# Optimization experiments

Hardware: AMD Instinct MI355X
Metric: run time of the kernel (lower is better)

Reference implementation:

```python
import jax, jax.numpy as jnp
import numpy as np


def setup_inputs() -> dict:
    key = jax.random.key(0)
    k1, k2, k3 = jax.random.split(key, 3)
    B, C, D, H, W = 4, 64, 32, 64, 64
    x = jax.random.normal(k1, (B, C, D, H, W), dtype=jnp.float32)
    # Conv3d(in=2, out=1, k=7), PyTorch default init: U(-s, s), s = 1/sqrt(fan_in)
    fan_in = 2 * 7 * 7 * 7
    s = 1.0 / np.sqrt(fan_in)
    conv_w = jax.random.uniform(k2, (1, 2, 7, 7, 7), dtype=jnp.float32, minval=-s, maxval=s)
    conv_b = jax.random.uniform(k3, (1,), dtype=jnp.float32, minval=-s, maxval=s)
    return {"x": x, "conv_w": conv_w, "conv_b": conv_b}


def reference(x, conv_w, conv_b):
    # channel-wise max and mean -> [B, 2, D, H, W]
    xc = jnp.stack([jnp.max(x, axis=1), jnp.mean(x, axis=1)], axis=1)
    # conv3d 2->1, k7, stride 1, padding 3 (SAME)
    y = jax.lax.conv_general_dilated(
        xc, conv_w,
        window_strides=(1, 1, 1),
        padding=[(3, 3), (3, 3), (3, 3)],
        dimension_numbers=("NCDHW", "OIDHW", "NCDHW"),
    ) + conv_b[None, :, None, None, None]
    scale = jax.nn.sigmoid(y)  # [B, 1, D, H, W]
    return x * scale
```

## Files before the change

kernel.cpp:

```cpp
#include <hip/hip_runtime.h>
#include <math.h>

#define B_ 4
#define C_ 64
#define D_ 32
#define H_ 64
#define W_ 64
#define S_ (D_*H_*W_)
#define S4_ (S_/4)

typedef float floatx4 __attribute__((ext_vector_type(4)));

__global__ __launch_bounds__(256) void reduce_kernel(const float* __restrict__ x,
                                                     float* __restrict__ xc) {
    int i  = blockIdx.x * 256 + threadIdx.x;
    int b  = i >> 15;
    int s4 = i & (S4_ - 1);
    const float4* x4 = reinterpret_cast<const float4*>(x) + (size_t)b * C_ * S4_ + s4;
    float4 v = x4[0];
    float mx0 = v.x, mx1 = v.y, mx2 = v.z, mx3 = v.w;
    float sm0 = v.x, sm1 = v.y, sm2 = v.z, sm3 = v.w;
    #pragma unroll 8
    for (int c = 1; c < C_; ++c) {
        float4 t = x4[(size_t)c * S4_];
        mx0 = fmaxf(mx0, t.x); sm0 += t.x;
        mx1 = fmaxf(mx1, t.y); sm1 += t.y;
        mx2 = fmaxf(mx2, t.z); sm2 += t.z;
        mx3 = fmaxf(mx3, t.w); sm3 += t.w;
    }
    float4* o = reinterpret_cast<float4*>(xc);
    float4 a; a.x = mx0; a.y = mx1; a.z = mx2; a.w = mx3;
    o[((size_t)b * 2 + 0) * S4_ + s4] = a;
    const float inv = 1.0f / 64.0f;
    float4 m; m.x = sm0 * inv; m.y = sm1 * inv; m.z = sm2 * inv; m.w = sm3 * inv;
    o[((size_t)b * 2 + 1) * S4_ + s4] = m;
}

#define YS 72
#define ZS (10*YS)
#define CHS (10*ZS)
__global__ __launch_bounds__(256) void conv_gate_kernel(const float* __restrict__ xc,
                                                        const float* __restrict__ x,
                                                        const float* __restrict__ cw,
                                                        const float* __restrict__ cb,
                                                        float* __restrict__ out) {
    __shared__ float tile[2 * CHS];
    __shared__ float wl[784];

    const int tid = threadIdx.x;
    const int b  = blockIdx.z >> 3;
    const int d0 = (blockIdx.z & 7) * 4;
    const int h0 = blockIdx.y * 4;

    const int w4 = tid & 15;
    const int hh = (tid >> 4) & 3;
    const int dd = tid >> 6;

    for (int idx = tid; idx < 784; idx += 256) {
        int ch = idx / 392;
        int r  = idx - ch * 392;
        int kz = r / 56;
        int r2 = r - kz * 56;
        int ky = r2 >> 3;
        int kw = r2 & 7;
        wl[idx] = (kw < 7) ? cw[ch * 343 + kz * 49 + ky * 7 + kw] : 0.f;
    }
    for (int idx = tid; idx < 2 * 10 * 10 * 70; idx += 256) {
        int ch = idx / 7000;
        int r  = idx - ch * 7000;
        int z  = r / 700;
        int r2 = r - z * 700;
        int y  = r2 / 70;
        int xw = r2 - y * 70;
        int gd = d0 + z - 3, gh = h0 + y - 3, gw = xw - 3;
        float v = 0.f;
        if ((unsigned)gd < (unsigned)D_ && (unsigned)gh < (unsigned)H_ &&
            (unsigned)gw < (unsigned)W_)
            v = xc[((size_t)(b * 2 + ch)) * S_ + gd * (H_ * W_) + gh * W_ + gw];
        tile[ch * CHS + z * ZS + y * YS + xw] = v;
    }
    __syncthreads();

    float acc0 = 0.f, acc1 = 0.f, acc2 = 0.f, acc3 = 0.f;
    for (int ch = 0; ch < 2; ++ch) {
        for (int kz = 0; kz < 7; ++kz) {
            const float* base = &tile[ch * CHS + (dd + kz) * ZS + hh * YS + w4 * 4];
            #pragma unroll
            for (int ky = 0; ky < 7; ++ky) {
                float4 f0 = *reinterpret_cast<const float4*>(base + ky * YS);
                float4 f1 = *reinterpret_cast<const float4*>(base + ky * YS + 4);
                float2 f2 = *reinterpret_cast<const float2*>(base + ky * YS + 8);
                float win[10] = {f0.x, f0.y, f0.z, f0.w, f1.x, f1.y, f1.z, f1.w, f2.x, f2.y};
                const float* wr = &wl[ch * 392 + kz * 56 + ky * 8];
                float4 wa = *reinterpret_cast<const float4*>(wr);
                float4 wb = *reinterpret_cast<const float4*>(wr + 4);
                float wt[7] = {wa.x, wa.y, wa.z, wa.w, wb.x, wb.y, wb.z};
                #pragma unroll
                for (int kw = 0; kw < 7; ++kw) {
                    acc0 = fmaf(win[kw + 0], wt[kw], acc0);
                    acc1 = fmaf(win[kw + 1], wt[kw], acc1);
                    acc2 = fmaf(win[kw + 2], wt[kw], acc2);
                    acc3 = fmaf(win[kw + 3], wt[kw], acc3);
                }
            }
        }
    }

    const float bias = cb[0];
    floatx4 s0;
    s0.x = 1.0f / (1.0f + __expf(-(acc0 + bias)));
    s0.y = 1.0f / (1.0f + __expf(-(acc1 + bias)));
    s0.z = 1.0f / (1.0f + __expf(-(acc2 + bias)));
    s0.w = 1.0f / (1.0f + __expf(-(acc3 + bias)));

    const int d = d0 + dd, h = h0 + hh, w = w4 * 4;
    const size_t sp = (size_t)d * (H_ * W_) + (size_t)h * W_ + w;
    const float* xp = x + (size_t)b * C_ * S_ + sp;
    float* op = out + (size_t)b * C_ * S_ + sp;
    #pragma unroll 8
    for (int c = 0; c < C_; ++c) {
        const size_t off = (size_t)c * S_;
        floatx4 xv = *reinterpret_cast<const floatx4*>(xp + off);
        *reinterpret_cast<floatx4*>(op + off) = xv * s0;
    }
}

extern "C" void kernel_launch(void* const* d_in, const int* in_sizes, int n_in,
                              void* d_out, int out_size, void* d_ws, size_t ws_size,
                              hipStream_t stream) {
    const float* x  = (const float*)d_in[0];
    const float* cw = (const float*)d_in[1];
    const float* cb = (const float*)d_in[2];
    float* out = (float*)d_out;
    float* xc  = (float*)d_ws;

    reduce_kernel<<<dim3((B_ * S4_) / 256), dim3(256), 0, stream>>>(x, xc);
    conv_gate_kernel<<<dim3(1, H_ / 4, B_ * (D_ / 4)), dim3(256), 0, stream>>>(
        xc, x, cw, cb, out);
}
```

Before: 93.54 us.

## Split conv and gating into separate kernels with grid-stride nontemporal gate

```diff
diff --git a/kernel.cpp b/kernel.cpp
--- a/kernel.cpp
+++ b/kernel.cpp
@@ -39,11 +39,10 @@
 #define YS 72
 #define ZS (10*YS)
 #define CHS (10*ZS)
-__global__ __launch_bounds__(256) void conv_gate_kernel(const float* __restrict__ xc,
-                                                        const float* __restrict__ x,
-                                                        const float* __restrict__ cw,
-                                                        const float* __restrict__ cb,
-                                                        float* __restrict__ out) {
+__global__ __launch_bounds__(256) void conv_kernel(const float* __restrict__ xc,
+                                                   const float* __restrict__ cw,
+                                                   const float* __restrict__ cb,
+                                                   float* __restrict__ scale) {
     __shared__ float tile[2 * CHS];
     __shared__ float wl[784];
 
@@ -114,14 +113,22 @@
     s0.w = 1.0f / (1.0f + __expf(-(acc3 + bias)));
 
     const int d = d0 + dd, h = h0 + hh, w = w4 * 4;
-    const size_t sp = (size_t)d * (H_ * W_) + (size_t)h * W_ + w;
-    const float* xp = x + (size_t)b * C_ * S_ + sp;
-    float* op = out + (size_t)b * C_ * S_ + sp;
-    #pragma unroll 8
-    for (int c = 0; c < C_; ++c) {
-        const size_t off = (size_t)c * S_;
-        floatx4 xv = *reinterpret_cast<const floatx4*>(xp + off);
-        *reinterpret_cast<floatx4*>(op + off) = xv * s0;
+    *reinterpret_cast<floatx4*>(
+        &scale[(size_t)b * S_ + (size_t)d * (H_ * W_) + (size_t)h * W_ + w]) = s0;
+}
+
+#define GATE_BLOCKS 2048
+__global__ __launch_bounds__(256) void gate_kernel(const float* __restrict__ x,
+                                                   const float* __restrict__ scale,
+                                                   float* __restrict__ out) {
+    const size_t total = (size_t)B_ * C_ * S4_;
+    const size_t stride = (size_t)GATE_BLOCKS * 256;
+    for (size_t i = (size_t)blockIdx.x * 256 + threadIdx.x; i < total; i += stride) {
+        int b  = (int)(i >> 21);
+        int s4 = (int)(i & (S4_ - 1));
+        floatx4 xv = reinterpret_cast<const floatx4*>(x)[i];
+        floatx4 sv = reinterpret_cast<const floatx4*>(scale)[(size_t)b * S4_ + s4];
+        __builtin_nontemporal_store(xv * sv, reinterpret_cast<floatx4*>(out) + i);
     }
 }
 
@@ -131,10 +138,11 @@
     const float* x  = (const float*)d_in[0];
     const float* cw = (const float*)d_in[1];
     const float* cb = (const float*)d_in[2];
-    float* out = (float*)d_out;
-    float* xc  = (float*)d_ws;
+    float* out   = (float*)d_out;
+    float* xc    = (float*)d_ws;
+    float* scale = xc + (size_t)B_ * 2 * S_;
 
     reduce_kernel<<<dim3((B_ * S4_) / 256), dim3(256), 0, stream>>>(x, xc);
-    conv_gate_kernel<<<dim3(1, H_ / 4, B_ * (D_ / 4)), dim3(256), 0, stream>>>(
-        xc, x, cw, cb, out);
+    conv_kernel<<<dim3(1, H_ / 4, B_ * (D_ / 4)), dim3(256), 0, stream>>>(xc, cw, cb, scale);
+    gate_kernel<<<dim3(GATE_BLOCKS), dim3(256), 0, stream>>>(x, scale, out);
 }
```

Measured after the change: 114.0 us. 1.22x slower.

## Halve conv block depth and stage one channel at a time in LDS

Applied to the files above, without the earlier changes.

```diff
diff --git a/kernel.cpp b/kernel.cpp
--- a/kernel.cpp
+++ b/kernel.cpp
@@ -36,27 +36,26 @@
     o[((size_t)b * 2 + 1) * S4_ + s4] = m;
 }
 
-#define YS 72
-#define ZS (10*YS)
-#define CHS (10*ZS)
-__global__ __launch_bounds__(256) void conv_gate_kernel(const float* __restrict__ xc,
+#define HYS 72
+#define HZS (10*HYS)
+__global__ __launch_bounds__(128) void conv_gate_kernel(const float* __restrict__ xc,
                                                         const float* __restrict__ x,
                                                         const float* __restrict__ cw,
                                                         const float* __restrict__ cb,
                                                         float* __restrict__ out) {
-    __shared__ float tile[2 * CHS];
+    __shared__ float tile[8 * HZS];
     __shared__ float wl[784];
 
     const int tid = threadIdx.x;
-    const int b  = blockIdx.z >> 3;
-    const int d0 = (blockIdx.z & 7) * 4;
+    const int b  = blockIdx.z >> 4;
+    const int d0 = (blockIdx.z & 15) * 2;
     const int h0 = blockIdx.y * 4;
 
     const int w4 = tid & 15;
     const int hh = (tid >> 4) & 3;
     const int dd = tid >> 6;
 
-    for (int idx = tid; idx < 784; idx += 256) {
+    for (int idx = tid; idx < 784; idx += 128) {
         int ch = idx / 392;
         int r  = idx - ch * 392;
         int kz = r / 56;
@@ -65,35 +64,34 @@
         int kw = r2 & 7;
         wl[idx] = (kw < 7) ? cw[ch * 343 + kz * 49 + ky * 7 + kw] : 0.f;
     }
-    for (int idx = tid; idx < 2 * 10 * 10 * 70; idx += 256) {
-        int ch = idx / 7000;
-        int r  = idx - ch * 7000;
-        int z  = r / 700;
-        int r2 = r - z * 700;
-        int y  = r2 / 70;
-        int xw = r2 - y * 70;
-        int gd = d0 + z - 3, gh = h0 + y - 3, gw = xw - 3;
-        float v = 0.f;
-        if ((unsigned)gd < (unsigned)D_ && (unsigned)gh < (unsigned)H_ &&
-            (unsigned)gw < (unsigned)W_)
-            v = xc[((size_t)(b * 2 + ch)) * S_ + gd * (H_ * W_) + gh * W_ + gw];
-        tile[ch * CHS + z * ZS + y * YS + xw] = v;
-    }
-    __syncthreads();
 
     float acc0 = 0.f, acc1 = 0.f, acc2 = 0.f, acc3 = 0.f;
     for (int ch = 0; ch < 2; ++ch) {
+        for (int idx = tid; idx < 8 * 10 * 70; idx += 128) {
+            int z  = idx / 700;
+            int r2 = idx - z * 700;
+            int y  = r2 / 70;
+            int xw = r2 - y * 70;
+            int gd = d0 + z - 3, gh = h0 + y - 3, gw = xw - 3;
+            float v = 0.f;
+            if ((unsigned)gd < (unsigned)D_ && (unsigned)gh < (unsigned)H_ &&
+                (unsigned)gw < (unsigned)W_)
+                v = xc[((size_t)(b * 2 + ch)) * S_ + gd * (H_ * W_) + gh * W_ + gw];
+            tile[z * HZS + y * HYS + xw] = v;
+        }
+        __syncthreads();
+
         for (int kz = 0; kz < 7; ++kz) {
-            const float* base = &tile[ch * CHS + (dd + kz) * ZS + hh * YS + w4 * 4];
+            const float* base = &tile[(dd + kz) * HZS + hh * HYS + w4 * 4];
+            const float* wch  = &wl[ch * 392 + kz * 56];
             #pragma unroll
             for (int ky = 0; ky < 7; ++ky) {
-                float4 f0 = *reinterpret_cast<const float4*>(base + ky * YS);
-                float4 f1 = *reinterpret_cast<const float4*>(base + ky * YS + 4);
-                float2 f2 = *reinterpret_cast<const float2*>(base + ky * YS + 8);
+                float4 f0 = *reinterpret_cast<const float4*>(base + ky * HYS);
+                float4 f1 = *reinterpret_cast<const float4*>(base + ky * HYS + 4);
+                float2 f2 = *reinterpret_cast<const float2*>(base + ky * HYS + 8);
                 float win[10] = {f0.x, f0.y, f0.z, f0.w, f1.x, f1.y, f1.z, f1.w, f2.x, f2.y};
-                const float* wr = &wl[ch * 392 + kz * 56 + ky * 8];
-                float4 wa = *reinterpret_cast<const float4*>(wr);
-                float4 wb = *reinterpret_cast<const float4*>(wr + 4);
+                float4 wa = *reinterpret_cast<const float4*>(wch + ky * 8);
+                float4 wb = *reinterpret_cast<const float4*>(wch + ky * 8 + 4);
                 float wt[7] = {wa.x, wa.y, wa.z, wa.w, wb.x, wb.y, wb.z};
                 #pragma unroll
                 for (int kw = 0; kw < 7; ++kw) {
@@ -104,6 +102,7 @@
                 }
             }
         }
+        __syncthreads();
     }
 
     const float bias = cb[0];
@@ -135,6 +134,6 @@
     float* xc  = (float*)d_ws;
 
     reduce_kernel<<<dim3((B_ * S4_) / 256), dim3(256), 0, stream>>>(x, xc);
-    conv_gate_kernel<<<dim3(1, H_ / 4, B_ * (D_ / 4)), dim3(256), 0, stream>>>(
+    conv_gate_kernel<<<dim3(1, H_ / 4, B_ * (D_ / 2)), dim3(128), 0, stream>>>(
         xc, x, cw, cb, out);
 }
```

Result: slower. 102.5 us (+9.5%).
